# Performance work log

Hardware: AMD Instinct MI355X
Metric: run time of the kernel (lower is better)

Reference implementation:

```python
import jax, jax.numpy as jnp
import numpy as np

N, R, E = 20000, 4, 40000
C_IN, C_EDGE, HID, OUT = 256, 128, 512, 256
H = 8
D = HID // H
SCALE = 1.0 / float(np.sqrt(D))


def _hgt_layer(x, src, dst, Wkqv, bkqv, Wk, Wv, prel, Wout, bout, skip):
    # x: [n, c_in]; src/dst: [R, E] int; Wk/Wv: [R, H, D, D]; prel: [R, H]
    n = x.shape[0]
    kqv = x @ Wkqv + bkqv                      # [n, 3*HID], split order k|q|v (torch.tensor_split)
    k, q, v = jnp.split(kqv, 3, axis=1)
    k = k.reshape(n, H, D)
    q = q.reshape(n, H, D)
    v = v.reshape(n, H, D)
    # per-(relation, head) DxD transforms (HeteroLinear k_rel / v_rel, no bias)
    k_rel = jnp.einsum('nhd,rhde->rnhe', k, Wk)   # [R, n, H, D]
    v_rel = jnp.einsum('nhd,rhde->rnhe', v, Wv)
    gather = jax.vmap(lambda t, i: t[i])          # per-relation gather
    k_e = gather(k_rel, src)                      # [R, E, H, D]
    v_e = gather(v_rel, src)
    q_e = q[dst]                                  # [R, E, H, D]
    alpha = jnp.einsum('rehd,rehd->reh', q_e, k_e) * prel[:, None, :] * SCALE
    m = src.shape[0] * src.shape[1]
    alpha = alpha.reshape(m, H)
    dstf = dst.reshape(m)
    # segment softmax over destination nodes, jointly across all relations
    amax = jax.ops.segment_max(alpha, dstf, num_segments=n)      # [n, H]
    ae = jnp.exp(alpha - amax[dstf])
    denom = jax.ops.segment_sum(ae, dstf, num_segments=n)
    w = ae / (denom[dstf] + 1e-16)
    msg = (v_e.reshape(m, H, D) * w[:, :, None]).reshape(m, H * D)
    agg = jax.ops.segment_sum(msg, dstf, num_segments=n)          # [n, HID]
    out = jax.nn.gelu(agg, approximate=False) @ Wout + bout
    if skip is not None:  # sigmoid-gated residual, only when dims match
        a = jax.nn.sigmoid(skip)
        out = a * out + (1.0 - a) * x
    return out


def setup_inputs() -> dict:
    key = jax.random.key(0)
    ks = jax.random.split(key, 16)
    def g(k, shape, fan):
        return jax.random.normal(k, shape, jnp.float32) / np.sqrt(fan)
    inp = {
        'x': jax.random.normal(ks[0], (N, C_IN), jnp.float32),
        'edge_index': jax.random.randint(ks[1], (R, 2, E), 0, N),
        'edge_attr': jax.random.normal(ks[2], (R, E, C_EDGE), jnp.float32),
        'Wkqv0': g(ks[3], (C_IN, 3 * HID), C_IN), 'bkqv0': jnp.zeros((3 * HID,), jnp.float32),
        'Wk0': g(ks[4], (R, H, D, D), D), 'Wv0': g(ks[5], (R, H, D, D), D),
        'prel0': jnp.ones((R, H), jnp.float32),
        'Wout0': g(ks[6], (HID, HID), HID), 'bout0': jnp.zeros((HID,), jnp.float32),
        'Wkqv1': g(ks[7], (HID, 3 * HID), HID), 'bkqv1': jnp.zeros((3 * HID,), jnp.float32),
        'Wk1': g(ks[8], (R, H, D, D), D), 'Wv1': g(ks[9], (R, H, D, D), D),
        'prel1': jnp.ones((R, H), jnp.float32),
        'Wout1': g(ks[10], (HID, HID), HID), 'bout1': jnp.zeros((HID,), jnp.float32),
        'skip1': jnp.ones((), jnp.float32),
        'Wfc': g(ks[11], (HID, OUT), HID), 'bfc': jnp.zeros((OUT,), jnp.float32),
        'We1': g(ks[12], (C_EDGE, HID), C_EDGE), 'be1': jnp.zeros((HID,), jnp.float32),
        'We2': g(ks[13], (HID, OUT), HID), 'be2': jnp.zeros((OUT,), jnp.float32),
    }
    return inp


def reference(x, edge_index, edge_attr, Wkqv0, bkqv0, Wk0, Wv0, prel0, Wout0, bout0, Wkqv1, bkqv1, Wk1, Wv1, prel1, Wout1, bout1, skip1, Wfc, bfc, We1, be1, We2, be2):
    src = edge_index[:, 0, :]
    dst = edge_index[:, 1, :]
    h = _hgt_layer(x, src, dst, Wkqv0, bkqv0, Wk0, Wv0, prel0, Wout0, bout0, None)
    h = _hgt_layer(h, src, dst, Wkqv1, bkqv1, Wk1, Wv1, prel1, Wout1, bout1, skip1)
    node_embeds = h @ Wfc + bfc
    e = edge_attr.reshape(R * E, C_EDGE)  # concat over relations
    edge_embeds = jax.nn.relu(e @ We1 + be1) @ We2 + be2
    return node_embeds, edge_embeds
```

## Files before the change

kernel.cpp:

```cpp
#include <hip/hip_runtime.h>
#include <cstdint>
#include <cstddef>

#define NN      20000
#define RR      4
#define EE      40000
#define CIN     256
#define CEDGE   128
#define HIDW    512
#define OUTW    256
#define NH      8
#define MEDGE   (RR*EE)
#define SCALEF  0.125f

typedef unsigned short u16;
typedef short s8v  __attribute__((ext_vector_type(8)));
typedef float f32x4 __attribute__((ext_vector_type(4)));

#define B_KQV   10240000ull
#define B_KREL  71680000ull
#define B_AGG   153600000ull
#define B_H0    174080000ull
#define B_H1    194560000ull
#define B_ALPHA 215040000ull
#define B_LSE   220160000ull
#define B_ROWP  220800000ull
#define B_EREC  220880128ull
#define B_WTS   221520128ull
#define WS_NEED 227000000ull

#define SZH ((size_t)NN * 256)

__device__ __forceinline__ u16 f2b(float f) {
    unsigned u = __float_as_uint(f);
    unsigned r = (u + 0x7FFFu + ((u >> 16) & 1u)) >> 16;
    return (u16)r;
}
__device__ __forceinline__ float b2f(u16 h) { return __uint_as_float(((unsigned)h) << 16); }
__device__ __forceinline__ float gelu_exact(float x) {
    return 0.5f * x * (1.0f + erff(x * 0.70710678118654752f));
}

__device__ __forceinline__ void gl_lds16(const u16* g, u16* l) {
    __builtin_amdgcn_global_load_lds(
        (const __attribute__((address_space(1))) void*)g,
        (__attribute__((address_space(3))) void*)l, 16, 0, 0);
}

template<int BN, int ACT, bool OUTBF16, bool BIAS, bool SKIP, bool AF32 = false>
__global__ __launch_bounds__(256) void gemm_bf16(
    const void* __restrict__ Av, int lda, size_t astride,
    const u16* __restrict__ BT, int ldb, size_t bstride,
    const float* __restrict__ bias,
    void* __restrict__ Cv, int ldc, size_t cstride,
    int M, int K,
    const u16* __restrict__ skipx, const float* __restrict__ gatep)
{
    constexpr int FN = BN / 32;
    constexpr int BI = BN / 32;
    __shared__ __align__(16) u16 As[128 * 64];
    __shared__ __align__(16) u16 Bs[BN * 64];

    const int t = threadIdx.x, lane = t & 63, wid = t >> 6;
    const int m0 = blockIdx.y * 128, n0 = blockIdx.x * BN;
    const int z  = blockIdx.z;
    const u16*   Bz = BT + (size_t)z * bstride;
    const float* Af = (const float*)Av + (AF32 ? (size_t)z * astride : 0);
    const u16*   Au = (const u16*)Av   + (AF32 ? 0 : (size_t)z * astride);
    const int wm = wid >> 1, wn = wid & 1;

    const int srow   = lane >> 3;
    const int schunk = (lane & 7) ^ srow;

    f32x4 acc[4][FN];
    #pragma unroll
    for (int i = 0; i < 4; ++i)
        #pragma unroll
        for (int j = 0; j < FN; ++j)
            acc[i][j] = (f32x4){0.f, 0.f, 0.f, 0.f};

    for (int k0 = 0; k0 < K; k0 += 64) {
        if (AF32) {
            #pragma unroll
            for (int i = 0; i < 4; ++i) {
                int c = i * 256 + t;
                int row = c >> 3, cc = c & 7;
                int gr = m0 + row; gr = gr < M ? gr : M - 1;
                const float* Ap = Af + (size_t)gr * lda + k0 + cc * 8;
                float4 p = *(const float4*)Ap;
                float4 q = *(const float4*)(Ap + 4);
                s8v v;
                v[0] = (short)f2b(p.x); v[1] = (short)f2b(p.y);
                v[2] = (short)f2b(p.z); v[3] = (short)f2b(p.w);
                v[4] = (short)f2b(q.x); v[5] = (short)f2b(q.y);
                v[6] = (short)f2b(q.z); v[7] = (short)f2b(q.w);
                *(s8v*)&As[row * 64 + ((cc ^ (row & 7)) << 3)] = v;
            }
        } else {
            #pragma unroll
            for (int i = 0; i < 4; ++i) {
                int t4 = wid * 4 + i;
                int row = t4 * 8 + srow;
                int gr = m0 + row; gr = gr < M ? gr : M - 1;
                gl_lds16(Au + (size_t)gr * lda + k0 + schunk * 8, &As[t4 * 512]);
            }
        }
        #pragma unroll
        for (int i = 0; i < BI; ++i) {
            int tb = wid * BI + i;
            int col = n0 + tb * 8 + srow;
            gl_lds16(Bz + (size_t)col * ldb + k0 + schunk * 8, &Bs[tb * 512]);
        }
        __syncthreads();
        #pragma unroll
        for (int ks = 0; ks < 2; ++ks) {
            s8v af[4], bf[FN];
            #pragma unroll
            for (int i = 0; i < 4; ++i) {
                int arow = wm * 64 + i * 16 + (lane & 15);
                int ac   = (ks * 4 + (lane >> 4)) ^ (lane & 7);
                af[i] = *(const s8v*)&As[arow * 64 + ac * 8];
            }
            #pragma unroll
            for (int j = 0; j < FN; ++j) {
                int brow = wn * (BN / 2) + j * 16 + (lane & 15);
                int bc   = (ks * 4 + (lane >> 4)) ^ (lane & 7);
                bf[j] = *(const s8v*)&Bs[brow * 64 + bc * 8];
            }
            #pragma unroll
            for (int i = 0; i < 4; ++i)
                #pragma unroll
                for (int j = 0; j < FN; ++j)
                    acc[i][j] = __builtin_amdgcn_mfma_f32_16x16x32_bf16(af[i], bf[j], acc[i][j], 0, 0, 0);
        }
        __syncthreads();
    }

    float gate = 1.f, ogate = 0.f;
    if (SKIP) { float s = *gatep; gate = 1.f / (1.f + expf(-s)); ogate = 1.f - gate; }
    u16*   Cb = (u16*)Cv   + (size_t)z * cstride;
    float* Cf = (float*)Cv + (size_t)z * cstride;
    #pragma unroll
    for (int i = 0; i < 4; ++i) {
        int rbase = m0 + wm * 64 + i * 16 + (lane >> 4) * 4;
        #pragma unroll
        for (int j = 0; j < FN; ++j) {
            int col = n0 + wn * (BN / 2) + j * 16 + (lane & 15);
            float bv = BIAS ? bias[col] : 0.f;
            #pragma unroll
            for (int q = 0; q < 4; ++q) {
                int r = rbase + q;
                if (r >= M) continue;
                float v = acc[i][j][q] + bv;
                if (ACT == 1) v = fmaxf(v, 0.f);
                if (ACT == 2) v = gelu_exact(v);
                if (SKIP) v = gate * v + ogate * b2f(skipx[(size_t)r * ldc + col]);
                if (OUTBF16) Cb[(size_t)r * ldc + col] = f2b(v);
                else         Cf[(size_t)r * ldc + col] = v;
            }
        }
    }
}

__global__ __launch_bounds__(256) void edge_mlp(
    const float* __restrict__ ea, const u16* __restrict__ We1T,
    const float* __restrict__ b1, const u16* __restrict__ We2T,
    const float* __restrict__ b2, float* __restrict__ out)
{
    __shared__ __align__(16) u16 Ae[64 * 128];
    __shared__ __align__(16) u16 Ic[64 * 128];

    const int t = threadIdx.x, lane = t & 63, w = t >> 6;
    const int e0 = blockIdx.x * 64;
    const int l15 = lane & 15, l4 = lane >> 4;

    #pragma unroll
    for (int i = 0; i < 4; ++i) {
        int c = i * 256 + t;
        int row = c >> 4, cc = c & 15;
        const float* Ap = ea + (size_t)(e0 + row) * 128 + cc * 8;
        float4 p = *(const float4*)Ap;
        float4 q = *(const float4*)(Ap + 4);
        s8v v;
        v[0] = (short)f2b(p.x); v[1] = (short)f2b(p.y);
        v[2] = (short)f2b(p.z); v[3] = (short)f2b(p.w);
        v[4] = (short)f2b(q.x); v[5] = (short)f2b(q.y);
        v[6] = (short)f2b(q.z); v[7] = (short)f2b(q.w);
        *(s8v*)&Ae[row * 128 + ((cc ^ (row & 7)) << 3)] = v;
    }
    __syncthreads();

    f32x4 acc2[4][4];
    #pragma unroll
    for (int m = 0; m < 4; ++m)
        #pragma unroll
        for (int n = 0; n < 4; ++n)
            acc2[m][n] = (f32x4){0.f, 0.f, 0.f, 0.f};

    for (int c = 0; c < 4; ++c) {
        f32x4 sacc[4][2];
        #pragma unroll
        for (int m = 0; m < 4; ++m)
            #pragma unroll
            for (int n = 0; n < 2; ++n)
                sacc[m][n] = (f32x4){0.f, 0.f, 0.f, 0.f};
        #pragma unroll
        for (int ks = 0; ks < 4; ++ks) {
            s8v af[4], bf[2];
            #pragma unroll
            for (int m = 0; m < 4; ++m) {
                int row = m * 16 + l15;
                int kc  = (ks * 4 + l4) ^ (row & 7);
                af[m] = *(const s8v*)&Ae[row * 128 + kc * 8];
            }
            #pragma unroll
            for (int n = 0; n < 2; ++n) {
                int col1 = c * 128 + w * 32 + n * 16 + l15;
                bf[n] = *(const s8v*)(We1T + (size_t)col1 * 128 + ks * 32 + l4 * 8);
            }
            #pragma unroll
            for (int m = 0; m < 4; ++m)
                #pragma unroll
                for (int n = 0; n < 2; ++n)
                    sacc[m][n] = __builtin_amdgcn_mfma_f32_16x16x32_bf16(af[m], bf[n], sacc[m][n], 0, 0, 0);
        }
        __syncthreads();
        #pragma unroll
        for (int m = 0; m < 4; ++m) {
            #pragma unroll
            for (int n = 0; n < 2; ++n) {
                int col = w * 32 + n * 16 + l15;
                float bv = b1[c * 128 + col];
                #pragma unroll
                for (int q = 0; q < 4; ++q) {
                    int row = m * 16 + l4 * 4 + q;
                    float v = fmaxf(sacc[m][n][q] + bv, 0.f);
                    Ic[row * 128 + (((col >> 3) ^ (row & 7)) << 3) + (col & 7)] = f2b(v);
                }
            }
        }
        __syncthreads();
        #pragma unroll
        for (int ks = 0; ks < 4; ++ks) {
            s8v af[4], bf[4];
            #pragma unroll
            for (int m = 0; m < 4; ++m) {
                int row = m * 16 + l15;
                int kc  = (ks * 4 + l4) ^ (row & 7);
                af[m] = *(const s8v*)&Ic[row * 128 + kc * 8];
            }
            #pragma unroll
            for (int n = 0; n < 4; ++n) {
                int col = w * 64 + n * 16 + l15;
                bf[n] = *(const s8v*)(We2T + (size_t)col * 512 + c * 128 + ks * 32 + l4 * 8);
            }
            #pragma unroll
            for (int m = 0; m < 4; ++m)
                #pragma unroll
                for (int n = 0; n < 4; ++n)
                    acc2[m][n] = __builtin_amdgcn_mfma_f32_16x16x32_bf16(af[m], bf[n], acc2[m][n], 0, 0, 0);
        }
    }

    #pragma unroll
    for (int m = 0; m < 4; ++m) {
        #pragma unroll
        for (int n = 0; n < 4; ++n) {
            int col = w * 64 + n * 16 + l15;
            float bv = b2[col];
            #pragma unroll
            for (int q = 0; q < 4; ++q) {
                int row = m * 16 + l4 * 4 + q;
                out[(size_t)(e0 + row) * 256 + col] = acc2[m][n][q] + bv;
            }
        }
    }
}

__global__ __launch_bounds__(256) void transpose_f2b(
    const float* __restrict__ W, u16* __restrict__ WT, int K, int N)
{
    __shared__ float tile[32][33];
    int kb = blockIdx.x * 32, nb = blockIdx.y * 32;
    int tx = threadIdx.x & 31, ty = threadIdx.x >> 5;
    #pragma unroll
    for (int i = 0; i < 32; i += 8)
        tile[ty + i][tx] = W[(size_t)(kb + ty + i) * N + nb + tx];
    __syncthreads();
    #pragma unroll
    for (int i = 0; i < 32; i += 8)
        WT[(size_t)(nb + ty + i) * K + kb + tx] = f2b(tile[tx][ty + i]);
}

__global__ void conv_wk(const float* __restrict__ Wk, u16* __restrict__ WkT)
{
    int idx = blockIdx.x * 256 + threadIdx.x;
    if (idx >= 8 * 256 * 64) return;
    int d = idx & 63, re = (idx >> 6) & 255, h = idx >> 14;
    int e = re & 63, r = re >> 6;
    WkT[idx] = f2b(Wk[(size_t)(((r * 8 + h) * 64 + d) * 64) + e]);
}

__global__ void conv_wv(const float* __restrict__ Wv, u16* __restrict__ WvT)
{
    int idx = blockIdx.x * 256 + threadIdx.x;
    if (idx >= 8 * 64 * 256) return;
    int d = idx & 63, r = (idx >> 6) & 3, e = (idx >> 8) & 63, h = idx >> 14;
    WvT[idx] = f2b(Wv[(size_t)(((r * 8 + h) * 64 + d) * 64) + e]);
}

__global__ void deg_kernel(const int* __restrict__ ei, int* __restrict__ rowptr)
{
    int idx = blockIdx.x * 256 + threadIdx.x;
    if (idx >= MEDGE) return;
    int r = idx / EE;
    atomicAdd(&rowptr[ei[idx + (r + 1) * EE]], 1);
}

__global__ __launch_bounds__(256) void scan_kernel(int* __restrict__ rowptr)
{
    __shared__ int buf[256];
    __shared__ int carry;
    const int t = threadIdx.x;
    if (t == 0) carry = 0;
    __syncthreads();
    for (int base = 0; base < NN; base += 256) {
        int i = base + t;
        int v = (i < NN) ? rowptr[i] : 0;
        buf[t] = v;
        __syncthreads();
        for (int off = 1; off < 256; off <<= 1) {
            int tv = (t >= off) ? buf[t - off] : 0;
            __syncthreads();
            buf[t] += tv;
            __syncthreads();
        }
        int total = buf[255];
        int excl = buf[t] - v;
        int c = carry;
        __syncthreads();
        if (i < NN) rowptr[i] = c + excl;
        if (t == 0) carry = c + total;
        __syncthreads();
    }
    if (t == 0) rowptr[NN] = carry;
}

__global__ void fill_kernel(const int* __restrict__ ei, const int* __restrict__ rowptr,
                            int* __restrict__ fillcnt, int* __restrict__ erec)
{
    int idx = blockIdx.x * 256 + threadIdx.x;
    if (idx >= MEDGE) return;
    int r = idx / EE;
    int dst = ei[idx + (r + 1) * EE];
    int pos = rowptr[dst] + atomicAdd(&fillcnt[dst], 1);
    erec[pos] = idx;
}

__global__ __launch_bounds__(256) void alpha_stats(
    const u16* __restrict__ krel2, const u16* __restrict__ kqvb,
    const int* __restrict__ ei, const int* __restrict__ rowptr,
    const int* __restrict__ erec, const float* __restrict__ prel,
    float* __restrict__ alpha, float* __restrict__ lse)
{
    int n    = (blockIdx.x * 256 + threadIdx.x) >> 6;
    int lane = threadIdx.x & 63;
    if (n >= NN) return;
    int p0 = rowptr[n], p1 = rowptr[n + 1];
    int h = lane >> 3, sub = lane & 7;
    s8v qv = *(const s8v*)(kqvb + (size_t)n * 1536 + 512 + h * 64 + sub * 8);
    float qf[8];
    #pragma unroll
    for (int q = 0; q < 8; ++q) qf[q] = b2f((u16)qv[q]);
    float m = -3.0e38f, ssum = 0.f;
    for (int j = p0; j < p1; ++j) {
        int idx = erec[j];
        int r = idx / EE;
        int src = ei[idx + r * EE];
        s8v kv = *(const s8v*)(krel2 + (size_t)src * 2048 + h * 256 + r * 64 + sub * 8);
        float s = 0.f;
        #pragma unroll
        for (int q = 0; q < 8; ++q) s += b2f((u16)kv[q]) * qf[q];
        s += __shfl_xor(s, 1);
        s += __shfl_xor(s, 2);
        s += __shfl_xor(s, 4);
        float a = s * prel[r * NH + h] * SCALEF;
        if (sub == 0) alpha[(size_t)idx * 8 + h] = a;
        float mn = fmaxf(m, a);
        ssum = ssum * expf(m - mn) + expf(a - mn);
        m = mn;
    }
    if (sub == 0) lse[(size_t)n * 8 + h] = m + logf(ssum + 1e-16f);
}

__global__ __launch_bounds__(256) void wsum_all(
    const u16* __restrict__ kqvb, const float* __restrict__ alpha,
    const float* __restrict__ lse, const int* __restrict__ rowptr,
    const int* __restrict__ erec, const int* __restrict__ ei,
    u16* __restrict__ wsumH)
{
    int n    = (blockIdx.x * 256 + threadIdx.x) >> 6;
    int lane = threadIdx.x & 63;
    if (n >= NN) return;
    int p0 = rowptr[n], p1 = rowptr[n + 1];
    int h = lane >> 3;
    float ls = lse[(size_t)n * 8 + h];
    float a0[8] = {}, a1[8] = {}, a2[8] = {}, a3[8] = {};
    for (int j = p0; j < p1; ++j) {
        int idx = erec[j];
        int r = idx / EE;
        int src = ei[idx + r * EE];
        float w = expf(alpha[(size_t)idx * 8 + h] - ls);
        s8v vv = *(const s8v*)(kqvb + (size_t)src * 1536 + 1024 + lane * 8);
        if (r == 0) {
            #pragma unroll
            for (int q = 0; q < 8; ++q) a0[q] += w * b2f((u16)vv[q]);
        } else if (r == 1) {
            #pragma unroll
            for (int q = 0; q < 8; ++q) a1[q] += w * b2f((u16)vv[q]);
        } else if (r == 2) {
            #pragma unroll
            for (int q = 0; q < 8; ++q) a2[q] += w * b2f((u16)vv[q]);
        } else {
            #pragma unroll
            for (int q = 0; q < 8; ++q) a3[q] += w * b2f((u16)vv[q]);
        }
    }
    u16* base = wsumH + (size_t)h * SZH + (size_t)n * 256 + (lane & 7) * 8;
    s8v o;
    #pragma unroll
    for (int q = 0; q < 8; ++q) o[q] = (short)f2b(a0[q]);
    *(s8v*)(base + 0)   = o;
    #pragma unroll
    for (int q = 0; q < 8; ++q) o[q] = (short)f2b(a1[q]);
    *(s8v*)(base + 64)  = o;
    #pragma unroll
    for (int q = 0; q < 8; ++q) o[q] = (short)f2b(a2[q]);
    *(s8v*)(base + 128) = o;
    #pragma unroll
    for (int q = 0; q < 8; ++q) o[q] = (short)f2b(a3[q]);
    *(s8v*)(base + 192) = o;
}

extern "C" void kernel_launch(void* const* d_in, const int* in_sizes, int n_in,
                              void* d_out, int out_size, void* d_ws, size_t ws_size,
                              hipStream_t stream)
{
    const float* x    = (const float*)d_in[0];
    const int*   ei   = (const int*)d_in[1];
    const float* ea   = (const float*)d_in[2];
    const float* Wkqv[2] = {(const float*)d_in[3],  (const float*)d_in[10]};
    const float* bkqv[2] = {(const float*)d_in[4],  (const float*)d_in[11]};
    const float* Wk[2]   = {(const float*)d_in[5],  (const float*)d_in[12]};
    const float* Wv[2]   = {(const float*)d_in[6],  (const float*)d_in[13]};
    const float* prel[2] = {(const float*)d_in[7],  (const float*)d_in[14]};
    const float* Wout[2] = {(const float*)d_in[8],  (const float*)d_in[15]};
    const float* bout[2] = {(const float*)d_in[9],  (const float*)d_in[16]};
    const float* skip1 = (const float*)d_in[17];
    const float* Wfc   = (const float*)d_in[18];
    const float* bfc   = (const float*)d_in[19];
    const float* We1   = (const float*)d_in[20];
    const float* be1   = (const float*)d_in[21];
    const float* We2   = (const float*)d_in[22];
    const float* be2   = (const float*)d_in[23];

    if (ws_size < WS_NEED) return;

    char* wsb = (char*)d_ws;
    u16*   kqvb  = (u16*)(wsb + B_KQV);
    u16*   krel2 = (u16*)(wsb + B_KREL);
    u16*   wsumH = krel2;
    u16*   aggb  = (u16*)(wsb + B_AGG);
    u16*   h0b   = (u16*)(wsb + B_H0);
    u16*   h1b   = (u16*)(wsb + B_H1);
    float* alpha = (float*)(wsb + B_ALPHA);
    float* lse   = (float*)(wsb + B_LSE);
    int*   fillcnt = (int*)(wsb + B_LSE);
    int*   rowptr  = (int*)(wsb + B_ROWP);
    int*   erec    = (int*)(wsb + B_EREC);
    float* outf  = (float*)d_out;

    u16* wt = (u16*)(wsb + B_WTS);
    u16* WkqvT[2] = {wt, wt + 393216};              wt += 393216 + 786432;
    u16* WkT[2]   = {wt, wt + 131072};              wt += 262144;
    u16* WvT[2]   = {wt, wt + 131072};              wt += 262144;
    u16* WoutT[2] = {wt, wt + 262144};              wt += 524288;
    u16* WfcT     = wt;                             wt += 131072;
    u16* We1T     = wt;                             wt += 65536;
    u16* We2T     = wt;

    const dim3 blk(256);
    const int mt128  = (NN + 127) / 128;

    transpose_f2b<<<dim3(CIN / 32, 1536 / 32), blk, 0, stream>>>(Wkqv[0], WkqvT[0], CIN, 1536);
    transpose_f2b<<<dim3(HIDW / 32, 1536 / 32), blk, 0, stream>>>(Wkqv[1], WkqvT[1], HIDW, 1536);
    transpose_f2b<<<dim3(HIDW / 32, HIDW / 32), blk, 0, stream>>>(Wout[0], WoutT[0], HIDW, HIDW);
    transpose_f2b<<<dim3(HIDW / 32, HIDW / 32), blk, 0, stream>>>(Wout[1], WoutT[1], HIDW, HIDW);
    transpose_f2b<<<dim3(HIDW / 32, OUTW / 32), blk, 0, stream>>>(Wfc, WfcT, HIDW, OUTW);
    transpose_f2b<<<dim3(CEDGE / 32, HIDW / 32), blk, 0, stream>>>(We1, We1T, CEDGE, HIDW);
    transpose_f2b<<<dim3(HIDW / 32, OUTW / 32), blk, 0, stream>>>(We2, We2T, HIDW, OUTW);
    for (int l = 0; l < 2; ++l) {
        conv_wk<<<(131072 + 255) / 256, blk, 0, stream>>>(Wk[l], WkT[l]);
        conv_wv<<<(131072 + 255) / 256, blk, 0, stream>>>(Wv[l], WvT[l]);
    }

    hipMemsetAsync(rowptr, 0, (NN + 1) * sizeof(int), stream);
    hipMemsetAsync(fillcnt, 0, NN * sizeof(int), stream);
    deg_kernel<<<(MEDGE + 255) / 256, blk, 0, stream>>>(ei, rowptr);
    scan_kernel<<<1, blk, 0, stream>>>(rowptr);
    fill_kernel<<<(MEDGE + 255) / 256, blk, 0, stream>>>(ei, rowptr, fillcnt, erec);

    for (int l = 0; l < 2; ++l) {
        int K = (l == 0) ? CIN : HIDW;

        if (l == 0)
            gemm_bf16<128, 0, true, true, false, true><<<dim3(12, mt128), blk, 0, stream>>>(
                (const void*)x, K, 0, WkqvT[0], K, 0, bkqv[0], kqvb, 1536, 0, NN, K, nullptr, nullptr);
        else
            gemm_bf16<128, 0, true, true, false><<<dim3(12, mt128), blk, 0, stream>>>(
                (const void*)h0b, K, 0, WkqvT[1], K, 0, bkqv[1], kqvb, 1536, 0, NN, K, nullptr, nullptr);

        gemm_bf16<128, 0, true, false, false><<<dim3(2, mt128, NH), blk, 0, stream>>>(
            (const void*)kqvb, 1536, 64, WkT[l], 64, (size_t)256 * 64, nullptr,
            krel2, 2048, 256, NN, 64, nullptr, nullptr);

        alpha_stats<<<(NN * 64) / 256, blk, 0, stream>>>(
            krel2, kqvb, ei, rowptr, erec, prel[l], alpha, lse);

        wsum_all<<<(NN * 64) / 256, blk, 0, stream>>>(
            kqvb, alpha, lse, rowptr, erec, ei, wsumH);

        gemm_bf16<64, 2, true, false, false><<<dim3(1, mt128, NH), blk, 0, stream>>>(
            (const void*)wsumH, 256, SZH, WvT[l], 256, (size_t)64 * 256, nullptr,
            aggb, 512, 64, NN, 256, nullptr, nullptr);

        if (l == 0)
            gemm_bf16<128, 0, true, true, false><<<dim3(4, mt128), blk, 0, stream>>>(
                (const void*)aggb, 512, 0, WoutT[0], 512, 0, bout[0], h0b, 512, 0, NN, 512, nullptr, nullptr);
        else
            gemm_bf16<128, 0, true, true, true><<<dim3(4, mt128), blk, 0, stream>>>(
                (const void*)aggb, 512, 0, WoutT[1], 512, 0, bout[1], h1b, 512, 0, NN, 512, h0b, skip1);
    }

    gemm_bf16<128, 0, false, true, false><<<dim3(2, mt128), blk, 0, stream>>>(
        (const void*)h1b, 512, 0, WfcT, 512, 0, bfc, outf, 256, 0, NN, 512, nullptr, nullptr);

    edge_mlp<<<MEDGE / 64, blk, 0, stream>>>(ea, We1T, be1, We2T, be2, outf + 5120000);
}
```

Baseline: 762.7 us.

## Double-buffer GEMM LDS tiles and prefetch edge-MLP weight fragments into registers

Measured after the change: 780.4 us. 1.02x slower.

```diff
diff --git a/kernel.cpp b/kernel.cpp
--- a/kernel.cpp
+++ b/kernel.cpp
@@ -47,19 +47,21 @@
         (__attribute__((address_space(3))) void*)l, 16, 0, 0);
 }
 
-template<int BN, int ACT, bool OUTBF16, bool BIAS, bool SKIP, bool AF32 = false>
+template<int BN, int K, int ACT, bool OUTBF16, bool BIAS, bool SKIP, bool AF32 = false>
 __global__ __launch_bounds__(256) void gemm_bf16(
     const void* __restrict__ Av, int lda, size_t astride,
     const u16* __restrict__ BT, int ldb, size_t bstride,
     const float* __restrict__ bias,
     void* __restrict__ Cv, int ldc, size_t cstride,
-    int M, int K,
+    int M,
     const u16* __restrict__ skipx, const float* __restrict__ gatep)
 {
     constexpr int FN = BN / 32;
     constexpr int BI = BN / 32;
-    __shared__ __align__(16) u16 As[128 * 64];
-    __shared__ __align__(16) u16 Bs[BN * 64];
+    constexpr int NT = K / 64;
+    constexpr int NB = (NT > 1) ? 2 : 1;
+    __shared__ __align__(16) u16 As[NB][128 * 64];
+    __shared__ __align__(16) u16 Bs[NB][BN * 64];
 
     const int t = threadIdx.x, lane = t & 63, wid = t >> 6;
     const int m0 = blockIdx.y * 128, n0 = blockIdx.x * BN;
@@ -72,68 +74,96 @@
     const int srow   = lane >> 3;
     const int schunk = (lane & 7) ^ srow;
 
-    f32x4 acc[4][FN];
-    #pragma unroll
-    for (int i = 0; i < 4; ++i)
-        #pragma unroll
-        for (int j = 0; j < FN; ++j)
-            acc[i][j] = (f32x4){0.f, 0.f, 0.f, 0.f};
-
-    for (int k0 = 0; k0 < K; k0 += 64) {
-        if (AF32) {
-            #pragma unroll
-            for (int i = 0; i < 4; ++i) {
-                int c = i * 256 + t;
-                int row = c >> 3, cc = c & 7;
-                int gr = m0 + row; gr = gr < M ? gr : M - 1;
-                const float* Ap = Af + (size_t)gr * lda + k0 + cc * 8;
-                float4 p = *(const float4*)Ap;
-                float4 q = *(const float4*)(Ap + 4);
-                s8v v;
-                v[0] = (short)f2b(p.x); v[1] = (short)f2b(p.y);
-                v[2] = (short)f2b(p.z); v[3] = (short)f2b(p.w);
-                v[4] = (short)f2b(q.x); v[5] = (short)f2b(q.y);
-                v[6] = (short)f2b(q.z); v[7] = (short)f2b(q.w);
-                *(s8v*)&As[row * 64 + ((cc ^ (row & 7)) << 3)] = v;
-            }
-        } else {
-            #pragma unroll
-            for (int i = 0; i < 4; ++i) {
-                int t4 = wid * 4 + i;
-                int row = t4 * 8 + srow;
-                int gr = m0 + row; gr = gr < M ? gr : M - 1;
-                gl_lds16(Au + (size_t)gr * lda + k0 + schunk * 8, &As[t4 * 512]);
-            }
-        }
+    float4 pa[4], qa[4];
+
+    auto stageA = [&](u16* dst, int k0) {
+        #pragma unroll
+        for (int i = 0; i < 4; ++i) {
+            int t4 = wid * 4 + i;
+            int row = t4 * 8 + srow;
+            int gr = m0 + row; gr = gr < M ? gr : M - 1;
+            gl_lds16(Au + (size_t)gr * lda + k0 + schunk * 8, dst + t4 * 512);
+        }
+    };
+    auto stageB = [&](u16* dst, int k0) {
         #pragma unroll
         for (int i = 0; i < BI; ++i) {
             int tb = wid * BI + i;
             int col = n0 + tb * 8 + srow;
-            gl_lds16(Bz + (size_t)col * ldb + k0 + schunk * 8, &Bs[tb * 512]);
-        }
-        __syncthreads();
+            gl_lds16(Bz + (size_t)col * ldb + k0 + schunk * 8, dst + tb * 512);
+        }
+    };
+    auto loadAf = [&](int k0) {
+        #pragma unroll
+        for (int i = 0; i < 4; ++i) {
+            int c = i * 256 + t;
+            int row = c >> 3, cc = c & 7;
+            int gr = m0 + row; gr = gr < M ? gr : M - 1;
+            const float* Ap = Af + (size_t)gr * lda + k0 + cc * 8;
+            pa[i] = *(const float4*)Ap;
+            qa[i] = *(const float4*)(Ap + 4);
+        }
+    };
+    auto writeAf = [&](u16* dst) {
+        #pragma unroll
+        for (int i = 0; i < 4; ++i) {
+            int c = i * 256 + t;
+            int row = c >> 3, cc = c & 7;
+            s8v v;
+            v[0] = (short)f2b(pa[i].x); v[1] = (short)f2b(pa[i].y);
+            v[2] = (short)f2b(pa[i].z); v[3] = (short)f2b(pa[i].w);
+            v[4] = (short)f2b(qa[i].x); v[5] = (short)f2b(qa[i].y);
+            v[6] = (short)f2b(qa[i].z); v[7] = (short)f2b(qa[i].w);
+            *(s8v*)&dst[row * 64 + ((cc ^ (row & 7)) << 3)] = v;
+        }
+    };
+
+    f32x4 acc[4][FN];
+    #pragma unroll
+    for (int i = 0; i < 4; ++i)
+        #pragma unroll
+        for (int j = 0; j < FN; ++j)
+            acc[i][j] = (f32x4){0.f, 0.f, 0.f, 0.f};
+
+    if (AF32) { loadAf(0); writeAf(As[0]); }
+    else      stageA(As[0], 0);
+    stageB(Bs[0], 0);
+    __syncthreads();
+
+    #pragma unroll
+    for (int tt = 0; tt < NT; ++tt) {
+        const int cur = tt & (NB - 1);
+        const int nxt = cur ^ (NB - 1);
+        s8v af[2][4], bf[2][FN];
         #pragma unroll
         for (int ks = 0; ks < 2; ++ks) {
-            s8v af[4], bf[FN];
             #pragma unroll
             for (int i = 0; i < 4; ++i) {
                 int arow = wm * 64 + i * 16 + (lane & 15);
                 int ac   = (ks * 4 + (lane >> 4)) ^ (lane & 7);
-                af[i] = *(const s8v*)&As[arow * 64 + ac * 8];
+                af[ks][i] = *(const s8v*)&As[cur][arow * 64 + ac * 8];
             }
             #pragma unroll
             for (int j = 0; j < FN; ++j) {
                 int brow = wn * (BN / 2) + j * 16 + (lane & 15);
                 int bc   = (ks * 4 + (lane >> 4)) ^ (lane & 7);
-                bf[j] = *(const s8v*)&Bs[brow * 64 + bc * 8];
-            }
+                bf[ks][j] = *(const s8v*)&Bs[cur][brow * 64 + bc * 8];
+            }
+        }
+        if (tt + 1 < NT) {
+            if (AF32) loadAf((tt + 1) * 64);
+            else      stageA(As[nxt], (tt + 1) * 64);
+            stageB(Bs[nxt], (tt + 1) * 64);
+        }
+        #pragma unroll
+        for (int ks = 0; ks < 2; ++ks)
             #pragma unroll
             for (int i = 0; i < 4; ++i)
                 #pragma unroll
                 for (int j = 0; j < FN; ++j)
-                    acc[i][j] = __builtin_amdgcn_mfma_f32_16x16x32_bf16(af[i], bf[j], acc[i][j], 0, 0, 0);
-        }
-        __syncthreads();
+                    acc[i][j] = __builtin_amdgcn_mfma_f32_16x16x32_bf16(af[ks][i], bf[ks][j], acc[i][j], 0, 0, 0);
+        if (AF32 && (tt + 1 < NT)) writeAf(As[nxt]);
+        if (tt + 1 < NT) __syncthreads();
     }
 
     float gate = 1.f, ogate = 0.f;
@@ -173,6 +203,30 @@
     const int t = threadIdx.x, lane = t & 63, w = t >> 6;
     const int e0 = blockIdx.x * 64;
     const int l15 = lane & 15, l4 = lane >> 4;
+
+    s8v w1f[4][2];
+    s8v w2f[2][4];
+
+    auto loadW1 = [&](int c) {
+        #pragma unroll
+        for (int ks = 0; ks < 4; ++ks)
+            #pragma unroll
+            for (int n = 0; n < 2; ++n) {
+                int col1 = c * 128 + w * 32 + n * 16 + l15;
+                w1f[ks][n] = *(const s8v*)(We1T + (size_t)col1 * 128 + ks * 32 + l4 * 8);
+            }
+    };
+    auto loadW2 = [&](int c) {
+        #pragma unroll
+        for (int ks = 0; ks < 2; ++ks)
+            #pragma unroll
+            for (int n = 0; n < 4; ++n) {
+                int col = w * 64 + n * 16 + l15;
+                w2f[ks][n] = *(const s8v*)(We2T + (size_t)col * 512 + c * 128 + ks * 32 + l4 * 8);
+            }
+    };
+
+    loadW1(0);
 
     #pragma unroll
     for (int i = 0; i < 4; ++i) {
@@ -197,7 +251,10 @@
         for (int n = 0; n < 4; ++n)
             acc2[m][n] = (f32x4){0.f, 0.f, 0.f, 0.f};
 
+    #pragma unroll
     for (int c = 0; c < 4; ++c) {
+        loadW2(c);
+
         f32x4 sacc[4][2];
         #pragma unroll
         for (int m = 0; m < 4; ++m)
@@ -206,7 +263,7 @@
                 sacc[m][n] = (f32x4){0.f, 0.f, 0.f, 0.f};
         #pragma unroll
         for (int ks = 0; ks < 4; ++ks) {
-            s8v af[4], bf[2];
+            s8v af[4];
             #pragma unroll
             for (int m = 0; m < 4; ++m) {
                 int row = m * 16 + l15;
@@ -214,15 +271,10 @@
                 af[m] = *(const s8v*)&Ae[row * 128 + kc * 8];
             }
             #pragma unroll
-            for (int n = 0; n < 2; ++n) {
-                int col1 = c * 128 + w * 32 + n * 16 + l15;
-                bf[n] = *(const s8v*)(We1T + (size_t)col1 * 128 + ks * 32 + l4 * 8);
-            }
-            #pragma unroll
             for (int m = 0; m < 4; ++m)
                 #pragma unroll
                 for (int n = 0; n < 2; ++n)
-                    sacc[m][n] = __builtin_amdgcn_mfma_f32_16x16x32_bf16(af[m], bf[n], sacc[m][n], 0, 0, 0);
+                    sacc[m][n] = __builtin_amdgcn_mfma_f32_16x16x32_bf16(af[m], w1f[ks][n], sacc[m][n], 0, 0, 0);
         }
         __syncthreads();
         #pragma unroll
@@ -239,10 +291,20 @@
                 }
             }
         }
+        if (c < 3) loadW1(c + 1);
         __syncthreads();
+
+        s8v w2g[2][4];
+        #pragma unroll
+        for (int k2 = 0; k2 < 2; ++k2)
+            #pragma unroll
+            for (int n = 0; n < 4; ++n) {
+                int col = w * 64 + n * 16 + l15;
+                w2g[k2][n] = *(const s8v*)(We2T + (size_t)col * 512 + c * 128 + (k2 + 2) * 32 + l4 * 8);
+            }
         #pragma unroll
         for (int ks = 0; ks < 4; ++ks) {
-            s8v af[4], bf[4];
+            s8v af[4];
             #pragma unroll
             for (int m = 0; m < 4; ++m) {
                 int row = m * 16 + l15;
@@ -250,15 +312,11 @@
                 af[m] = *(const s8v*)&Ic[row * 128 + kc * 8];
             }
             #pragma unroll
-            for (int n = 0; n < 4; ++n) {
-                int col = w * 64 + n * 16 + l15;
-                bf[n] = *(const s8v*)(We2T + (size_t)col * 512 + c * 128 + ks * 32 + l4 * 8);
-            }
-            #pragma unroll
             for (int m = 0; m < 4; ++m)
                 #pragma unroll
                 for (int n = 0; n < 4; ++n)
-                    acc2[m][n] = __builtin_amdgcn_mfma_f32_16x16x32_bf16(af[m], bf[n], acc2[m][n], 0, 0, 0);
+                    acc2[m][n] = __builtin_amdgcn_mfma_f32_16x16x32_bf16(
+                        af[m], (ks < 2) ? w2f[ks][n] : w2g[ks - 2][n], acc2[m][n], 0, 0, 0);
         }
     }
 
@@ -511,18 +569,16 @@
     fill_kernel<<<(MEDGE + 255) / 256, blk, 0, stream>>>(ei, rowptr, fillcnt, erec);
 
     for (int l = 0; l < 2; ++l) {
-        int K = (l == 0) ? CIN : HIDW;
-
         if (l == 0)
-            gemm_bf16<128, 0, true, true, false, true><<<dim3(12, mt128), blk, 0, stream>>>(
-                (const void*)x, K, 0, WkqvT[0], K, 0, bkqv[0], kqvb, 1536, 0, NN, K, nullptr, nullptr);
+            gemm_bf16<128, 256, 0, true, true, false, true><<<dim3(12, mt128), blk, 0, stream>>>(
+                (const void*)x, CIN, 0, WkqvT[0], CIN, 0, bkqv[0], kqvb, 1536, 0, NN, nullptr, nullptr);
         else
-            gemm_bf16<128, 0, true, true, false><<<dim3(12, mt128), blk, 0, stream>>>(
-                (const void*)h0b, K, 0, WkqvT[1], K, 0, bkqv[1], kqvb, 1536, 0, NN, K, nullptr, nullptr);
-
-        gemm_bf16<128, 0, true, false, false><<<dim3(2, mt128, NH), blk, 0, stream>>>(
+            gemm_bf16<128, 512, 0, true, true, false><<<dim3(12, mt128), blk, 0, stream>>>(
+                (const void*)h0b, HIDW, 0, WkqvT[1], HIDW, 0, bkqv[1], kqvb, 1536, 0, NN, nullptr, nullptr);
+
+        gemm_bf16<128, 64, 0, true, false, false><<<dim3(2, mt128, NH), blk, 0, stream>>>(
             (const void*)kqvb, 1536, 64, WkT[l], 64, (size_t)256 * 64, nullptr,
-            krel2, 2048, 256, NN, 64, nullptr, nullptr);
+            krel2, 2048, 256, NN, nullptr, nullptr);
 
         alpha_stats<<<(NN * 64) / 256, blk, 0, stream>>>(
             krel2, kqvb, ei, rowptr, erec, prel[l], alpha, lse);
@@ -530,20 +586,20 @@
         wsum_all<<<(NN * 64) / 256, blk, 0, stream>>>(
             kqvb, alpha, lse, rowptr, erec, ei, wsumH);
 
-        gemm_bf16<64, 2, true, false, false><<<dim3(1, mt128, NH), blk, 0, stream>>>(
+        gemm_bf16<64, 256, 2, true, false, false><<<dim3(1, mt128, NH), blk, 0, stream>>>(
             (const void*)wsumH, 256, SZH, WvT[l], 256, (size_t)64 * 256, nullptr,
-            aggb, 512, 64, NN, 256, nullptr, nullptr);
+            aggb, 512, 64, NN, nullptr, nullptr);
 
         if (l == 0)
-            gemm_bf16<128, 0, true, true, false><<<dim3(4, mt128), blk, 0, stream>>>(
-                (const void*)aggb, 512, 0, WoutT[0], 512, 0, bout[0], h0b, 512, 0, NN, 512, nullptr, nullptr);
+            gemm_bf16<128, 512, 0, true, true, false><<<dim3(4, mt128), blk, 0, stream>>>(
+                (const void*)aggb, 512, 0, WoutT[0], 512, 0, bout[0], h0b, 512, 0, NN, nullptr, nullptr);
         else
-            gemm_bf16<128, 0, true, true, true><<<dim3(4, mt128), blk, 0, stream>>>(
-                (const void*)aggb, 512, 0, WoutT[1], 512, 0, bout[1], h1b, 512, 0, NN, 512, h0b, skip1);
-    }
-
-    gemm_bf16<128, 0, false, true, false><<<dim3(2, mt128), blk, 0, stream>>>(
-        (const void*)h1b, 512, 0, WfcT, 512, 0, bfc, outf, 256, 0, NN, 512, nullptr, nullptr);
+            gemm_bf16<128, 512, 0, true, true, true><<<dim3(4, mt128), blk, 0, stream>>>(
+                (const void*)aggb, 512, 0, WoutT[1], 512, 0, bout[1], h1b, 512, 0, NN, h0b, skip1);
+    }
+
+    gemm_bf16<128, 512, 0, false, true, false><<<dim3(2, mt128), blk, 0, stream>>>(
+        (const void*)h1b, 512, 0, WfcT, 512, 0, bfc, outf, 256, 0, NN, nullptr, nullptr);
 
     edge_mlp<<<MEDGE / 64, blk, 0, stream>>>(ea, We1T, be1, We2T, be2, outf + 5120000);
 }
```
